# Optimization experiments

Measured on AMD Instinct MI355X. Metric: run time of the kernel, lower is better.

The kernel has to match this reference:

```python
import jax, jax.numpy as jnp
import numpy as np

N, D = 50000, 512


def setup_inputs() -> dict:
    key = jax.random.key(0)
    ks = jax.random.split(key, 8)
    s = 1.0 / np.sqrt(D)  # torch Linear default init scale
    return {
        "img_embed": jax.random.normal(ks[0], (N, D), dtype=jnp.float32),
        "ph_embed": jax.random.normal(ks[1], (N, D), dtype=jnp.float32),
        "W_shared": jax.random.uniform(ks[2], (D, D), jnp.float32, -s, s),
        "b_shared": jax.random.uniform(ks[3], (D,), jnp.float32, -s, s),
        "W_img": jax.random.uniform(ks[4], (D, D), jnp.float32, -s, s),
        "b_img": jax.random.uniform(ks[5], (D,), jnp.float32, -s, s),
        "W_ph": jax.random.uniform(ks[6], (D, D), jnp.float32, -s, s),
        "b_ph": jax.random.uniform(ks[7], (D,), jnp.float32, -s, s),
    }


def reference(img_embed, ph_embed, W_shared, b_shared, W_img, b_img, W_ph, b_ph):
    shared_embed = 0.5 * (img_embed + ph_embed)
    # torch Linear: x @ W.T + b
    img_att = jnp.tanh(jnp.einsum("nd,ed->ne", img_embed, W_img) + b_img)
    ph_att = jnp.tanh(jnp.einsum("nd,ed->ne", ph_embed, W_ph) + b_ph)
    shared_att = jnp.tanh(jnp.einsum("nd,ed->ne", shared_embed, W_shared) + b_shared)
    # trace(A @ A.T) == sum(A*A) (Frobenius norm squared) -- algebraic rewrite,
    # avoids the O(N^2 D) matmul in the original.
    shared_sq = jnp.sum(shared_att * shared_att)
    img_score = jnp.sum(img_att * img_att) / shared_sq
    ph_score = jnp.sum(ph_att * ph_att) / shared_sq
    w = jax.nn.softmax(jnp.stack([img_score, ph_score]))
    joint_embed = shared_att * shared_embed + img_att * img_embed + ph_att * ph_embed
    return joint_embed, w[0], w[1]
```

## Files before the change

kernel.cpp:

```cpp
#include <hip/hip_runtime.h>
#include <math.h>

#define N_ROWS 50000
#define DIM 512

#define BM 128
#define BN 64
#define BK 32
#define KSTEPS (DIM / BK)
#define N_STRIPS 391
#define STRIPS_PER_XCD 49
#define LDA 40
#define GRID_K2 (8 * STRIPS_PER_XCD * 8)
#define NSLOTS (GRID_K2 * 4)

typedef __attribute__((ext_vector_type(8))) short short8;
typedef __attribute__((ext_vector_type(4))) float float4v;

__device__ inline unsigned short f2bf(float x) {
    union { float f; unsigned u; } v; v.f = x;
    unsigned r = v.u + 0x7fffu + ((v.u >> 16) & 1u);
    return (unsigned short)(r >> 16);
}

__device__ inline short8 packv(float4v x, float4v y) {
    short8 r;
    r[0] = (short)f2bf(x[0]); r[1] = (short)f2bf(x[1]);
    r[2] = (short)f2bf(x[2]); r[3] = (short)f2bf(x[3]);
    r[4] = (short)f2bf(y[0]); r[5] = (short)f2bf(y[1]);
    r[6] = (short)f2bf(y[2]); r[7] = (short)f2bf(y[3]);
    return r;
}

__device__ inline float fast_tanh(float x) {
    float xc = fminf(fmaxf(x, -15.f), 15.f);
    float e = __expf(2.0f * xc);
    return 1.0f - 2.0f * __builtin_amdgcn_rcpf(e + 1.0f);
}

__global__ __launch_bounds__(256) void convert_w(
    const float* __restrict__ Wi, const float* __restrict__ Wp, const float* __restrict__ Ws,
    unsigned short* __restrict__ Wi_bf, unsigned short* __restrict__ Wp_bf,
    unsigned short* __restrict__ Ws_bf)
{
    const int t = blockIdx.x * 256 + threadIdx.x;
    const int mat = t >> 15;
    const size_t idx = (size_t)(t & 32767) * 8;
    const float* src = (mat == 0) ? Wi : ((mat == 1) ? Wp : Ws);
    unsigned short* dst = (mat == 0) ? Wi_bf : ((mat == 1) ? Wp_bf : Ws_bf);
    float4v a = *(const float4v*)(src + idx);
    float4v b = *(const float4v*)(src + idx + 4);
    *(short8*)(dst + idx) = packv(a, b);
}

__global__ __launch_bounds__(256, 2) void fused_all(
    const float* __restrict__ img, const float* __restrict__ ph,
    const unsigned short* __restrict__ Wi_bf, const unsigned short* __restrict__ Wp_bf,
    const unsigned short* __restrict__ Ws_bf,
    const float* __restrict__ bs, const float* __restrict__ bi, const float* __restrict__ bp,
    float* __restrict__ out, float* __restrict__ part)
{
    const int bid = blockIdx.x;
    const int tid = threadIdx.x;
    const int xcd = bid & 7;
    const int u   = bid >> 3;
    const int col = u & 7;
    const int s   = u >> 3;
    const int strip = xcd * STRIPS_PER_XCD + s;
    if (strip >= N_STRIPS) {
        if (tid < 4) {
            float4v z = {0.f, 0.f, 0.f, 0.f};
            *(float4v*)(part + ((size_t)bid * 4 + tid) * 4) = z;
        }
        return;
    }
    const int e0 = col * BN;
    const int n0 = strip * BM;

    __shared__ __align__(16) unsigned short sA[3][BM][LDA];
    __shared__ __align__(16) unsigned short sB[3][BN][LDA];

    const int lane = tid & 63;
    const int wid  = tid >> 6;
    const int wm   = wid & 1;
    const int wn   = wid >> 1;
    const int l15  = lane & 15;
    const int quad = lane >> 4;

    const int ar = tid >> 1;
    const int ah = tid & 1;
    const int arow = n0 + ar;
    const bool avalid = arow < N_ROWS;
    const size_t abase = (size_t)arow * DIM + ah * 16;
    const int br = tid >> 2;
    const int bc = (tid & 3) * 8;
    const size_t bbase = (size_t)(e0 + br) * DIM + bc;

    const unsigned short* Bmat[3] = { Wi_bf, Wp_bf, Ws_bf };

    float4v aI[4], aP[4];
    short8 bW[3];
#pragma unroll
    for (int q = 0; q < 4; ++q) { aI[q] = (float4v){0,0,0,0}; aP[q] = (float4v){0,0,0,0}; }

#define LOADK(k0_) do {                                                     \
        const int k0v = (k0_);                                              \
        if (avalid) {                                                       \
            const float* gi = img + abase + k0v;                            \
            const float* gp = ph  + abase + k0v;                            \
            aI[0] = *(const float4v*)(gi);      aI[1] = *(const float4v*)(gi + 4);  \
            aI[2] = *(const float4v*)(gi + 8);  aI[3] = *(const float4v*)(gi + 12); \
            aP[0] = *(const float4v*)(gp);      aP[1] = *(const float4v*)(gp + 4);  \
            aP[2] = *(const float4v*)(gp + 8);  aP[3] = *(const float4v*)(gp + 12); \
        }                                                                   \
        bW[0] = *(const short8*)(Bmat[0] + bbase + k0v);                    \
        bW[1] = *(const short8*)(Bmat[1] + bbase + k0v);                    \
        bW[2] = *(const short8*)(Bmat[2] + bbase + k0v);                    \
    } while (0)

    float4v acc[3][4][2];
#pragma unroll
    for (int m = 0; m < 3; ++m)
#pragma unroll
        for (int i = 0; i < 4; ++i)
#pragma unroll
            for (int j = 0; j < 2; ++j)
                acc[m][i][j] = (float4v){0.f, 0.f, 0.f, 0.f};

    LOADK(0);

#pragma unroll 1
    for (int kb = 0; kb < KSTEPS; ++kb) {
        asm volatile("" ::: "memory");
        __builtin_amdgcn_s_barrier();
        asm volatile("" ::: "memory");

        {
            float4v s0 = 0.5f * (aI[0] + aP[0]);
            float4v s1 = 0.5f * (aI[1] + aP[1]);
            float4v s2 = 0.5f * (aI[2] + aP[2]);
            float4v s3 = 0.5f * (aI[3] + aP[3]);
            *(short8*)&sA[0][ar][ah * 16]     = packv(aI[0], aI[1]);
            *(short8*)&sA[0][ar][ah * 16 + 8] = packv(aI[2], aI[3]);
            *(short8*)&sA[1][ar][ah * 16]     = packv(aP[0], aP[1]);
            *(short8*)&sA[1][ar][ah * 16 + 8] = packv(aP[2], aP[3]);
            *(short8*)&sA[2][ar][ah * 16]     = packv(s0, s1);
            *(short8*)&sA[2][ar][ah * 16 + 8] = packv(s2, s3);
            *(short8*)&sB[0][br][bc] = bW[0];
            *(short8*)&sB[1][br][bc] = bW[1];
            *(short8*)&sB[2][br][bc] = bW[2];
        }

        if (kb + 1 < KSTEPS) LOADK((kb + 1) * BK);

        asm volatile("s_waitcnt lgkmcnt(0)" ::: "memory");
        __builtin_amdgcn_s_barrier();
        asm volatile("" ::: "memory");

#pragma unroll
        for (int mat = 0; mat < 3; ++mat) {
            short8 a[4], b[2];
#pragma unroll
            for (int i = 0; i < 4; ++i)
                a[i] = *(const short8*)&sA[mat][wm * 64 + i * 16 + l15][quad * 8];
#pragma unroll
            for (int j = 0; j < 2; ++j)
                b[j] = *(const short8*)&sB[mat][wn * 32 + j * 16 + l15][quad * 8];
#pragma unroll
            for (int i = 0; i < 4; ++i)
#pragma unroll
                for (int j = 0; j < 2; ++j)
                    acc[mat][i][j] = __builtin_amdgcn_mfma_f32_16x16x32_bf16(
                        a[i], b[j], acc[mat][i][j], 0, 0, 0);
        }
    }
#undef LOADK

    float s_i = 0.f, s_p = 0.f, s_s = 0.f;
#pragma unroll
    for (int i = 0; i < 4; ++i) {
#pragma unroll
        for (int j = 0; j < 2; ++j) {
            const int c = e0 + wn * 32 + j * 16 + l15;
            const float bii = bi[c], bpp = bp[c], bss = bs[c];
            const int rbase = n0 + wm * 64 + i * 16 + quad * 4;
#pragma unroll
            for (int r = 0; r < 4; ++r) {
                const int nrow = rbase + r;
                const float ia = fast_tanh(acc[0][i][j][r] + bii);
                const float pa = fast_tanh(acc[1][i][j][r] + bpp);
                const float sa = fast_tanh(acc[2][i][j][r] + bss);
                if (nrow < N_ROWS) {
                    const size_t off = (size_t)nrow * DIM + c;
                    const float ie = img[off];
                    const float pe = ph[off];
                    const float se = 0.5f * (ie + pe);
                    out[off] = sa * se + ia * ie + pa * pe;
                    s_i += ia * ia; s_p += pa * pa; s_s += sa * sa;
                }
            }
        }
    }

#pragma unroll
    for (int off = 32; off > 0; off >>= 1) {
        s_i += __shfl_down(s_i, off);
        s_p += __shfl_down(s_p, off);
        s_s += __shfl_down(s_s, off);
    }
    if (lane == 0) {
        float4v v = {s_i, s_p, s_s, 0.f};
        *(float4v*)(part + ((size_t)bid * 4 + wid) * 4) = v;
    }
}

__global__ __launch_bounds__(256) void finalize(
    const float* __restrict__ part, float* __restrict__ wout)
{
    __shared__ float4v red[256];
    float4v acc = {0.f, 0.f, 0.f, 0.f};
    for (int i = threadIdx.x; i < NSLOTS; i += 256)
        acc += *(const float4v*)(part + (size_t)i * 4);
    red[threadIdx.x] = acc;
    __syncthreads();
    for (int s = 128; s > 0; s >>= 1) {
        if (threadIdx.x < s) red[threadIdx.x] += red[threadIdx.x + s];
        __syncthreads();
    }
    if (threadIdx.x == 0) {
        float4v t = red[0];
        const float inv_sh = 1.0f / t[2];
        const float is = t[0] * inv_sh;
        const float ps = t[1] * inv_sh;
        const float m  = fmaxf(is, ps);
        const float ei = expf(is - m), ep = expf(ps - m);
        const float inv = 1.0f / (ei + ep);
        wout[0] = ei * inv;
        wout[1] = ep * inv;
    }
}

extern "C" void kernel_launch(void* const* d_in, const int* in_sizes, int n_in,
                              void* d_out, int out_size, void* d_ws, size_t ws_size,
                              hipStream_t stream) {
    const float* img = (const float*)d_in[0];
    const float* ph  = (const float*)d_in[1];
    const float* Ws  = (const float*)d_in[2];
    const float* bs  = (const float*)d_in[3];
    const float* Wi  = (const float*)d_in[4];
    const float* bi  = (const float*)d_in[5];
    const float* Wp  = (const float*)d_in[6];
    const float* bp  = (const float*)d_in[7];
    float* out  = (float*)d_out;

    const size_t w_elems = (size_t)DIM * DIM;
    unsigned short* Wi_bf = (unsigned short*)((char*)d_ws + 256);
    unsigned short* Wp_bf = Wi_bf + w_elems;
    unsigned short* Ws_bf = Wp_bf + w_elems;
    float* part = (float*)((char*)d_ws + 256 + 3 * w_elems * sizeof(unsigned short));

    convert_w<<<384, 256, 0, stream>>>(Wi, Wp, Ws, Wi_bf, Wp_bf, Ws_bf);

    fused_all<<<GRID_K2, 256, 0, stream>>>(
        img, ph, Wi_bf, Wp_bf, Ws_bf, bs, bi, bp, out, part);

    finalize<<<1, 256, 0, stream>>>(part, out + (size_t)N_ROWS * DIM);
}
```

Baseline: 500.7 us.

## Compute shared matmul as sum of img and ph products; swizzle LDS stores

```diff
diff --git a/kernel.cpp b/kernel.cpp
--- a/kernel.cpp
+++ b/kernel.cpp
@@ -77,26 +77,27 @@
     const int e0 = col * BN;
     const int n0 = strip * BM;
 
-    __shared__ __align__(16) unsigned short sA[3][BM][LDA];
+    __shared__ __align__(16) unsigned short sA[2][BM][LDA];
     __shared__ __align__(16) unsigned short sB[3][BN][LDA];
 
     const int lane = tid & 63;
-    const int wid  = tid >> 6;
-    const int wm   = wid & 1;
-    const int wn   = wid >> 1;
+    const int wv   = tid >> 6;
+    const int wm   = wv & 1;
+    const int wn   = wv >> 1;
     const int l15  = lane & 15;
     const int quad = lane >> 4;
 
-    const int ar = tid >> 1;
-    const int ah = tid & 1;
+    const int la = lane >> 3;
+    const int lb = lane & 7;
+    const int ah = la & 1;
+    const int ar = wv * 32 + (((5 * (lb - 2 * ah)) & 7) + 8 * (la >> 1));
+    const int bc4 = la >> 1;
+    const int br  = wv * 16 + (((5 * (lb - bc4)) & 7) + 8 * (la & 1));
+
     const int arow = n0 + ar;
     const bool avalid = arow < N_ROWS;
     const size_t abase = (size_t)arow * DIM + ah * 16;
-    const int br = tid >> 2;
-    const int bc = (tid & 3) * 8;
-    const size_t bbase = (size_t)(e0 + br) * DIM + bc;
-
-    const unsigned short* Bmat[3] = { Wi_bf, Wp_bf, Ws_bf };
+    const size_t bbase = (size_t)(e0 + br) * DIM + bc4 * 8;
 
     float4v aI[4], aP[4];
     short8 bW[3];
@@ -113,14 +114,14 @@
             aP[0] = *(const float4v*)(gp);      aP[1] = *(const float4v*)(gp + 4);  \
             aP[2] = *(const float4v*)(gp + 8);  aP[3] = *(const float4v*)(gp + 12); \
         }                                                                   \
-        bW[0] = *(const short8*)(Bmat[0] + bbase + k0v);                    \
-        bW[1] = *(const short8*)(Bmat[1] + bbase + k0v);                    \
-        bW[2] = *(const short8*)(Bmat[2] + bbase + k0v);                    \
+        bW[0] = *(const short8*)(Wi_bf + bbase + k0v);                      \
+        bW[1] = *(const short8*)(Wp_bf + bbase + k0v);                      \
+        bW[2] = *(const short8*)(Ws_bf + bbase + k0v);                      \
     } while (0)
 
-    float4v acc[3][4][2];
-#pragma unroll
-    for (int m = 0; m < 3; ++m)
+    float4v acc[4][4][2];
+#pragma unroll
+    for (int m = 0; m < 4; ++m)
 #pragma unroll
         for (int i = 0; i < 4; ++i)
 #pragma unroll
@@ -135,21 +136,13 @@
         __builtin_amdgcn_s_barrier();
         asm volatile("" ::: "memory");
 
-        {
-            float4v s0 = 0.5f * (aI[0] + aP[0]);
-            float4v s1 = 0.5f * (aI[1] + aP[1]);
-            float4v s2 = 0.5f * (aI[2] + aP[2]);
-            float4v s3 = 0.5f * (aI[3] + aP[3]);
-            *(short8*)&sA[0][ar][ah * 16]     = packv(aI[0], aI[1]);
-            *(short8*)&sA[0][ar][ah * 16 + 8] = packv(aI[2], aI[3]);
-            *(short8*)&sA[1][ar][ah * 16]     = packv(aP[0], aP[1]);
-            *(short8*)&sA[1][ar][ah * 16 + 8] = packv(aP[2], aP[3]);
-            *(short8*)&sA[2][ar][ah * 16]     = packv(s0, s1);
-            *(short8*)&sA[2][ar][ah * 16 + 8] = packv(s2, s3);
-            *(short8*)&sB[0][br][bc] = bW[0];
-            *(short8*)&sB[1][br][bc] = bW[1];
-            *(short8*)&sB[2][br][bc] = bW[2];
-        }
+        *(short8*)&sA[0][ar][ah * 16]     = packv(aI[0], aI[1]);
+        *(short8*)&sA[0][ar][ah * 16 + 8] = packv(aI[2], aI[3]);
+        *(short8*)&sA[1][ar][ah * 16]     = packv(aP[0], aP[1]);
+        *(short8*)&sA[1][ar][ah * 16 + 8] = packv(aP[2], aP[3]);
+        *(short8*)&sB[0][br][bc4 * 8] = bW[0];
+        *(short8*)&sB[1][br][bc4 * 8] = bW[1];
+        *(short8*)&sB[2][br][bc4 * 8] = bW[2];
 
         if (kb + 1 < KSTEPS) LOADK((kb + 1) * BK);
 
@@ -157,21 +150,39 @@
         __builtin_amdgcn_s_barrier();
         asm volatile("" ::: "memory");
 
-#pragma unroll
-        for (int mat = 0; mat < 3; ++mat) {
-            short8 a[4], b[2];
-#pragma unroll
-            for (int i = 0; i < 4; ++i)
-                a[i] = *(const short8*)&sA[mat][wm * 64 + i * 16 + l15][quad * 8];
-#pragma unroll
-            for (int j = 0; j < 2; ++j)
-                b[j] = *(const short8*)&sB[mat][wn * 32 + j * 16 + l15][quad * 8];
-#pragma unroll
-            for (int i = 0; i < 4; ++i)
-#pragma unroll
-                for (int j = 0; j < 2; ++j)
-                    acc[mat][i][j] = __builtin_amdgcn_mfma_f32_16x16x32_bf16(
-                        a[i], b[j], acc[mat][i][j], 0, 0, 0);
+        short8 bI[2], bP[2], bS[2];
+#pragma unroll
+        for (int j = 0; j < 2; ++j) {
+            bI[j] = *(const short8*)&sB[0][wn * 32 + j * 16 + l15][quad * 8];
+            bP[j] = *(const short8*)&sB[1][wn * 32 + j * 16 + l15][quad * 8];
+            bS[j] = *(const short8*)&sB[2][wn * 32 + j * 16 + l15][quad * 8];
+        }
+        {
+            short8 a[4];
+#pragma unroll
+            for (int i = 0; i < 4; ++i)
+                a[i] = *(const short8*)&sA[0][wm * 64 + i * 16 + l15][quad * 8];
+#pragma unroll
+            for (int i = 0; i < 4; ++i)
+#pragma unroll
+                for (int j = 0; j < 2; ++j) {
+                    acc[0][i][j] = __builtin_amdgcn_mfma_f32_16x16x32_bf16(
+                        a[i], bI[j], acc[0][i][j], 0, 0, 0);
+                    acc[2][i][j] = __builtin_amdgcn_mfma_f32_16x16x32_bf16(
+                        a[i], bS[j], acc[2][i][j], 0, 0, 0);
+                }
+#pragma unroll
+            for (int i = 0; i < 4; ++i)
+                a[i] = *(const short8*)&sA[1][wm * 64 + i * 16 + l15][quad * 8];
+#pragma unroll
+            for (int i = 0; i < 4; ++i)
+#pragma unroll
+                for (int j = 0; j < 2; ++j) {
+                    acc[1][i][j] = __builtin_amdgcn_mfma_f32_16x16x32_bf16(
+                        a[i], bP[j], acc[1][i][j], 0, 0, 0);
+                    acc[3][i][j] = __builtin_amdgcn_mfma_f32_16x16x32_bf16(
+                        a[i], bS[j], acc[3][i][j], 0, 0, 0);
+                }
         }
     }
 #undef LOADK
@@ -189,7 +200,8 @@
                 const int nrow = rbase + r;
                 const float ia = fast_tanh(acc[0][i][j][r] + bii);
                 const float pa = fast_tanh(acc[1][i][j][r] + bpp);
-                const float sa = fast_tanh(acc[2][i][j][r] + bss);
+                const float sa = fast_tanh(
+                    0.5f * (acc[2][i][j][r] + acc[3][i][j][r]) + bss);
                 if (nrow < N_ROWS) {
                     const size_t off = (size_t)nrow * DIM + c;
                     const float ie = img[off];
@@ -210,7 +222,7 @@
     }
     if (lane == 0) {
         float4v v = {s_i, s_p, s_s, 0.f};
-        *(float4v*)(part + ((size_t)bid * 4 + wid) * 4) = v;
+        *(float4v*)(part + ((size_t)bid * 4 + wv) * 4) = v;
     }
 }
 
```

After: 563.9 us. 1.13x slower.
